# Performance work log

Hardware: AMD Instinct MI355X
Metric: run time of the kernel (lower is better)

Reference implementation:

```python
import jax, jax.numpy as jnp
import numpy as np

NUM_EXPERTS = 8
TOP_K = 2
HIDDEN = 768
FFN = 3072
B, S = 4, 4096


def setup_inputs() -> dict:
    key = jax.random.key(0)
    ks = jax.random.split(key, 7)
    scale_h = 1.0 / np.sqrt(HIDDEN)
    scale_f = 1.0 / np.sqrt(FFN)
    return {
        "hidden_states": jax.random.normal(ks[0], (B, S, HIDDEN), dtype=jnp.float32),
        "router_w": jax.random.normal(ks[1], (HIDDEN, NUM_EXPERTS), dtype=jnp.float32) * scale_h,
        "router_b": jnp.zeros((NUM_EXPERTS,), dtype=jnp.float32),
        "w1": jax.random.normal(ks[2], (NUM_EXPERTS, HIDDEN, FFN), dtype=jnp.float32) * scale_h,
        "b1": jnp.zeros((NUM_EXPERTS, FFN), dtype=jnp.float32),
        "w2": jax.random.normal(ks[3], (NUM_EXPERTS, FFN, HIDDEN), dtype=jnp.float32) * scale_f,
        "b2": jnp.zeros((NUM_EXPERTS, HIDDEN), dtype=jnp.float32),
    }


def _moe_forward(x_flat, router_w, router_b, w1, b1, w2, b2):
    T = x_flat.shape[0]
    # Router: logits [T, E]
    router_logits = x_flat @ router_w + router_b
    routing_weights = jax.nn.softmax(router_logits, axis=-1)
    # Top-k gating: softmax over the selected top-k logits
    top_vals, top_idx = jax.lax.top_k(router_logits, TOP_K)
    top_gates = jax.nn.softmax(top_vals, axis=-1)
    # Scatter gates into dense dispatch mask [T, E]
    rows = jnp.arange(T)[:, None]
    dispatch_mask = jnp.zeros_like(routing_weights).at[rows, top_idx].set(top_gates)
    # Expert computation: combined = sum_e gate[:, e] * FFN_e(x)
    # (tokens with zero gate contribute exactly 0, matching the torch scatter-combine)
    combined = jnp.zeros_like(x_flat)
    for e in range(NUM_EXPERTS):
        h = jax.nn.gelu(x_flat @ w1[e] + b1[e])  # [T, FFN]
        y = h @ w2[e] + b2[e]                    # [T, HIDDEN]
        combined = combined + dispatch_mask[:, e:e + 1] * y
    # Auxiliary load-balancing loss
    mean_routing_prob = jnp.mean(routing_weights, axis=0)
    tokens_per_expert = jnp.sum(dispatch_mask, axis=0) / T
    aux_loss = jnp.sum(mean_routing_prob * tokens_per_expert) * NUM_EXPERTS
    return combined, routing_weights, dispatch_mask, aux_loss, router_logits


def reference(hidden_states, router_w, router_b, w1, b1, w2, b2):
    batch, seq, hid = hidden_states.shape
    x_flat = hidden_states.reshape(-1, hid)
    combined, routing_weights, dispatch_mask, aux_loss, router_logits = _moe_forward(
        x_flat, router_w, router_b, w1, b1, w2, b2)
    E = NUM_EXPERTS
    return (
        combined.reshape(batch, seq, hid),            # expert_outputs
        routing_weights.reshape(batch, seq, E),       # routing_weights
        dispatch_mask.reshape(batch, seq, E),         # dispatch_mask
        aux_loss,                                     # aux_loss
        router_logits.reshape(batch, seq, E),         # router_logits
    )
```

## Files before the change

kernel.cpp:

```cpp
#include <hip/hip_runtime.h>
#include <math.h>

#define TOKENS 16384
#define HID 768
#define FFN_DIM 3072
#define NEXP 8
#define MAX_TILES 264

#define RT_TPB 128
#define RT_BLOCKS (TOKENS / RT_TPB)

typedef __bf16 bf16x8 __attribute__((ext_vector_type(8)));
typedef float f32x4 __attribute__((ext_vector_type(4)));

#define GLOBAL_AS(p) ((const __attribute__((address_space(1))) void*)(p))
#define LDS_AS(p)    ((__attribute__((address_space(3))) void*)(p))

__device__ __forceinline__ float gelu_f(float x) {
    const float x3 = x * x * x;
    const float z = 0.7978845608028654f * (x + 0.044715f * x3);
    const float e = __expf(2.f * z);
    const float t = 1.f - 2.f / (e + 1.f);
    return 0.5f * x * (1.f + t);
}

__device__ __forceinline__ unsigned short f2bf(float v) {
    return __builtin_bit_cast(unsigned short, (__bf16)v);
}

__global__ void __launch_bounds__(512) router_kernel(
    const float* __restrict__ x, const float* __restrict__ rw,
    const float* __restrict__ rb,
    float* __restrict__ out_rw, float* __restrict__ out_dm,
    float* __restrict__ out_logits,
    int* __restrict__ counts, float* __restrict__ probsum,
    float* __restrict__ gatesum, int* __restrict__ lists,
    float* __restrict__ glists)
{
    __shared__ int s_cnt[NEXP], s_base[NEXP];
    __shared__ float s_prob[NEXP], s_gate[NEXP];
    __shared__ int s_e1[RT_TPB], s_s1[RT_TPB], s_e2[RT_TPB], s_s2[RT_TPB];
    __shared__ float s_g1v[RT_TPB], s_g2v[RT_TPB];

    const int tid = threadIdx.x;
    if (tid < NEXP) { s_cnt[tid] = 0; s_prob[tid] = 0.f; s_gate[tid] = 0.f; }
    __syncthreads();

    const int wave = tid >> 6, lane = tid & 63;

    for (int it = 0; it < RT_TPB / 8; ++it) {
        const int lt = wave * (RT_TPB / 8) + it;
        const int t = blockIdx.x * RT_TPB + lt;
        const float* xr = x + (size_t)t * HID;
        float acc[NEXP];
#pragma unroll
        for (int e = 0; e < NEXP; ++e) acc[e] = 0.f;
#pragma unroll
        for (int j = 0; j < 12; ++j) {
            const int i = lane + (j << 6);
            const float xv = xr[i];
            const float4 a = ((const float4*)(rw + (size_t)i * NEXP))[0];
            const float4 b = ((const float4*)(rw + (size_t)i * NEXP))[1];
            acc[0] += xv * a.x; acc[1] += xv * a.y; acc[2] += xv * a.z; acc[3] += xv * a.w;
            acc[4] += xv * b.x; acc[5] += xv * b.y; acc[6] += xv * b.z; acc[7] += xv * b.w;
        }
#pragma unroll
        for (int off = 32; off > 0; off >>= 1)
#pragma unroll
            for (int e = 0; e < NEXP; ++e) acc[e] += __shfl_down(acc[e], off, 64);

        if (lane == 0) {
            float lg[NEXP];
            float m = -1e30f;
#pragma unroll
            for (int e = 0; e < NEXP; ++e) { lg[e] = acc[e] + rb[e]; m = fmaxf(m, lg[e]); }
            float ex[NEXP]; float s = 0.f;
#pragma unroll
            for (int e = 0; e < NEXP; ++e) { ex[e] = expf(lg[e] - m); s += ex[e]; }
            const float inv = 1.f / s;
            float* lrow = out_logits + (size_t)t * NEXP;
            float* prow = out_rw + (size_t)t * NEXP;
#pragma unroll
            for (int e = 0; e < NEXP; ++e) {
                lrow[e] = lg[e];
                const float p = ex[e] * inv;
                prow[e] = p;
                atomicAdd(&s_prob[e], p);
            }
            int i1 = 0;
#pragma unroll
            for (int e = 1; e < NEXP; ++e) if (lg[e] > lg[i1]) i1 = e;
            int i2 = (i1 == 0) ? 1 : 0;
#pragma unroll
            for (int e = 0; e < NEXP; ++e) if (e != i1 && lg[e] > lg[i2]) i2 = e;
            const float e2 = expf(lg[i2] - lg[i1]);
            const float g1 = 1.f / (1.f + e2);
            const float g2 = e2 / (1.f + e2);
            out_dm[(size_t)t * NEXP + i1] = g1;
            out_dm[(size_t)t * NEXP + i2] = g2;
            atomicAdd(&s_gate[i1], g1);
            atomicAdd(&s_gate[i2], g2);
            s_e1[lt] = i1; s_s1[lt] = atomicAdd(&s_cnt[i1], 1); s_g1v[lt] = g1;
            s_e2[lt] = i2; s_s2[lt] = atomicAdd(&s_cnt[i2], 1); s_g2v[lt] = g2;
        }
    }
    __syncthreads();
    if (tid < NEXP) {
        s_base[tid] = atomicAdd(&counts[tid], s_cnt[tid]);
        atomicAdd(&probsum[tid], s_prob[tid]);
        atomicAdd(&gatesum[tid], s_gate[tid]);
    }
    __syncthreads();
    if (tid < RT_TPB) {
        const int t = blockIdx.x * RT_TPB + tid;
        int e = s_e1[tid]; int p = s_base[e] + s_s1[tid];
        lists[e * TOKENS + p] = t; glists[e * TOKENS + p] = s_g1v[tid];
        e = s_e2[tid]; p = s_base[e] + s_s2[tid];
        lists[e * TOKENS + p] = t; glists[e * TOKENS + p] = s_g2v[tid];
    }
}

__global__ void finalize_kernel(const int* __restrict__ counts,
                                const float* __restrict__ probsum,
                                const float* __restrict__ gatesum,
                                int* __restrict__ poffs,
                                float* __restrict__ out_aux)
{
    if (threadIdx.x == 0 && blockIdx.x == 0) {
        float s = 0.f; int po = 0;
        for (int e = 0; e < NEXP; ++e) {
            poffs[e] = po;
            po += ((counts[e] + 127) >> 7) << 7;
            s += (probsum[e] / (float)TOKENS) * (gatesum[e] / (float)TOKENS);
        }
        poffs[NEXP] = po;
        *out_aux = s * (float)NEXP;
    }
}

__global__ void __launch_bounds__(192) gatherx_kernel(
    const float* __restrict__ x, const int* __restrict__ counts,
    const int* __restrict__ poffs, const int* __restrict__ lists,
    unsigned short* __restrict__ Xg)
{
    const int r = blockIdx.x;
    if (r >= poffs[NEXP]) return;
    int e = 0;
#pragma unroll
    for (int q = 1; q < NEXP; ++q) e += (r >= poffs[q]);
    const int ri = r - poffs[e];
    const int tid = threadIdx.x;
    uint2 o = make_uint2(0u, 0u);
    if (ri < counts[e]) {
        const int tok = lists[e * TOKENS + ri];
        const float4 v = *(const float4*)&x[(size_t)tok * HID + tid * 4];
        o.x = (unsigned)f2bf(v.x) | ((unsigned)f2bf(v.y) << 16);
        o.y = (unsigned)f2bf(v.z) | ((unsigned)f2bf(v.w) << 16);
    }
    *(uint2*)&Xg[(size_t)r * HID + tid * 4] = o;
}

__global__ void __launch_bounds__(256) convT_kernel(const float* __restrict__ in,
                                                    unsigned short* __restrict__ out,
                                                    int R, int C)
{
    __shared__ float sT[32][65];
    const int e = blockIdx.z;
    const float* in_e = in + (size_t)e * R * C;
    unsigned short* out_e = out + (size_t)e * R * C;
    const int r0 = blockIdx.y * 64;
    const int c0 = blockIdx.x * 32;
    const int tid = threadIdx.x;
    const int rr = tid >> 3, c4 = (tid & 7) * 4;
#pragma unroll
    for (int half = 0; half < 2; ++half) {
        const int r = rr + half * 32;
        const float4 v = *(const float4*)&in_e[(size_t)(r0 + r) * C + c0 + c4];
        sT[c4 + 0][r] = v.x; sT[c4 + 1][r] = v.y;
        sT[c4 + 2][r] = v.z; sT[c4 + 3][r] = v.w;
    }
    __syncthreads();
    const int c = tid >> 3, u = tid & 7;
    uint4 pk;
    const float* sr = &sT[c][u * 8];
    pk.x = (unsigned)f2bf(sr[0]) | ((unsigned)f2bf(sr[1]) << 16);
    pk.y = (unsigned)f2bf(sr[2]) | ((unsigned)f2bf(sr[3]) << 16);
    pk.z = (unsigned)f2bf(sr[4]) | ((unsigned)f2bf(sr[5]) << 16);
    pk.w = (unsigned)f2bf(sr[6]) | ((unsigned)f2bf(sr[7]) << 16);
    *(uint4*)&out_e[(size_t)(c0 + c) * R + r0 + u * 8] = pk;
}

__global__ void __launch_bounds__(256) gemm1_kernel(
    const unsigned short* __restrict__ Xg, const unsigned short* __restrict__ W1T,
    const float* __restrict__ b1, const int* __restrict__ poffs,
    unsigned short* __restrict__ H, int grBase, int tilesPG)
{
    const int mtile = blockIdx.x;
    if (mtile >= tilesPG) return;
    const int gr = grBase + mtile * 128;
    if (gr >= poffs[NEXP]) return;
    int e = 0;
#pragma unroll
    for (int q = 1; q < NEXP; ++q) e += (gr >= poffs[q]);
    const int hbase = gr - grBase;
    const int n0 = blockIdx.y * 128;

    __shared__ __bf16 sA[128 * 64];
    __shared__ __bf16 sB[128 * 64];

    const int tid = threadIdx.x;
    const int w = tid >> 6, lane = tid & 63;

    const unsigned short* w1e = W1T + (size_t)e * (FFN_DIM * HID);
    const int lr = lane >> 3;
    const int lk = (lane & 7) * 8;
    const unsigned short* aPtr[4];
    const unsigned short* bPtr[4];
    __bf16* ldsA[4];
    __bf16* ldsB[4];
#pragma unroll
    for (int j = 0; j < 4; ++j) {
        const int row = (w * 4 + j) * 8 + lr;
        aPtr[j] = Xg + (size_t)(gr + row) * HID + lk;
        bPtr[j] = w1e + (size_t)(n0 + row) * HID + lk;
        ldsA[j] = sA + (w * 4 + j) * 512;
        ldsB[j] = sB + (w * 4 + j) * 512;
    }

    f32x4 acc[4][4];
#pragma unroll
    for (int a = 0; a < 4; ++a)
#pragma unroll
        for (int b = 0; b < 4; ++b) acc[a][b] = (f32x4)(0.f);

    const int wm = (w >> 1) * 64, wn = (w & 1) * 64;
    const int fr = lane & 15;
    const int fk = (lane >> 4) * 8;

    for (int kt = 0; kt < HID / 64; ++kt) {
        const int k0 = kt * 64;
#pragma unroll
        for (int j = 0; j < 4; ++j) {
            __builtin_amdgcn_global_load_lds(GLOBAL_AS(aPtr[j] + k0), LDS_AS(ldsA[j]), 16, 0, 0);
            __builtin_amdgcn_global_load_lds(GLOBAL_AS(bPtr[j] + k0), LDS_AS(ldsB[j]), 16, 0, 0);
        }
        __syncthreads();
#pragma unroll
        for (int kk = 0; kk < 64; kk += 32) {
            bf16x8 af[4], bb[4];
#pragma unroll
            for (int t = 0; t < 4; ++t) {
                af[t] = *(const bf16x8*)&sA[(wm + t * 16 + fr) * 64 + kk + fk];
                bb[t] = *(const bf16x8*)&sB[(wn + t * 16 + fr) * 64 + kk + fk];
            }
#pragma unroll
            for (int tm = 0; tm < 4; ++tm)
#pragma unroll
                for (int tn = 0; tn < 4; ++tn)
                    acc[tm][tn] = __builtin_amdgcn_mfma_f32_16x16x32_bf16(
                        af[tm], bb[tn], acc[tm][tn], 0, 0, 0);
        }
        __syncthreads();
    }

    const float* b1e = b1 + (size_t)e * FFN_DIM;
    float bias[4];
#pragma unroll
    for (int tn = 0; tn < 4; ++tn) bias[tn] = b1e[n0 + wn + tn * 16 + fr];
#pragma unroll
    for (int tm = 0; tm < 4; ++tm) {
#pragma unroll
        for (int tn = 0; tn < 4; ++tn) {
            const int n = n0 + wn + tn * 16 + fr;
#pragma unroll
            for (int r = 0; r < 4; ++r) {
                const int mloc = wm + tm * 16 + (lane >> 4) * 4 + r;
                const float h = gelu_f(acc[tm][tn][r] + bias[tn]);
                H[(size_t)(hbase + mloc) * FFN_DIM + n] = f2bf(h);
            }
        }
    }
}

__global__ void __launch_bounds__(256) gemm2_kernel(
    const unsigned short* __restrict__ H, const unsigned short* __restrict__ W2T,
    const float* __restrict__ b2, const int* __restrict__ counts,
    const int* __restrict__ poffs, const int* __restrict__ lists,
    const float* __restrict__ glists, float* __restrict__ out,
    int grBase, int tilesPG)
{
    const int mtile = blockIdx.x;
    if (mtile >= tilesPG) return;
    const int gr = grBase + mtile * 128;
    if (gr >= poffs[NEXP]) return;
    int e = 0;
#pragma unroll
    for (int q = 1; q < NEXP; ++q) e += (gr >= poffs[q]);
    const int cnt = counts[e];
    const int m0 = gr - poffs[e];
    const int hbase = gr - grBase;
    const int n0 = blockIdx.y * 128;

    __shared__ __bf16 sA[128 * 64];
    __shared__ __bf16 sB[128 * 64];
    __shared__ int sTok[128];
    __shared__ float sGate[128];

    const int tid = threadIdx.x;
    const int w = tid >> 6, lane = tid & 63;
    if (tid < 128) {
        int ri = m0 + tid; if (ri > cnt - 1) ri = cnt - 1;
        sTok[tid] = lists[e * TOKENS + ri];
        sGate[tid] = glists[e * TOKENS + ri];
    }

    const unsigned short* w2e = W2T + (size_t)e * (FFN_DIM * HID);
    const int lr = lane >> 3;
    const int lk = (lane & 7) * 8;
    const unsigned short* aPtr[4];
    const unsigned short* bPtr[4];
    __bf16* ldsA[4];
    __bf16* ldsB[4];
#pragma unroll
    for (int j = 0; j < 4; ++j) {
        const int row = (w * 4 + j) * 8 + lr;
        aPtr[j] = H + (size_t)(hbase + row) * FFN_DIM + lk;
        bPtr[j] = w2e + (size_t)(n0 + row) * FFN_DIM + lk;
        ldsA[j] = sA + (w * 4 + j) * 512;
        ldsB[j] = sB + (w * 4 + j) * 512;
    }

    f32x4 acc[4][4];
#pragma unroll
    for (int a = 0; a < 4; ++a)
#pragma unroll
        for (int b = 0; b < 4; ++b) acc[a][b] = (f32x4)(0.f);

    const int wm = (w >> 1) * 64, wn = (w & 1) * 64;
    const int fr = lane & 15;
    const int fk = (lane >> 4) * 8;

    for (int kt = 0; kt < FFN_DIM / 64; ++kt) {
        const int k0 = kt * 64;
#pragma unroll
        for (int j = 0; j < 4; ++j) {
            __builtin_amdgcn_global_load_lds(GLOBAL_AS(aPtr[j] + k0), LDS_AS(ldsA[j]), 16, 0, 0);
            __builtin_amdgcn_global_load_lds(GLOBAL_AS(bPtr[j] + k0), LDS_AS(ldsB[j]), 16, 0, 0);
        }
        __syncthreads();
#pragma unroll
        for (int kk = 0; kk < 64; kk += 32) {
            bf16x8 af[4], bb[4];
#pragma unroll
            for (int t = 0; t < 4; ++t) {
                af[t] = *(const bf16x8*)&sA[(wm + t * 16 + fr) * 64 + kk + fk];
                bb[t] = *(const bf16x8*)&sB[(wn + t * 16 + fr) * 64 + kk + fk];
            }
#pragma unroll
            for (int tm = 0; tm < 4; ++tm)
#pragma unroll
                for (int tn = 0; tn < 4; ++tn)
                    acc[tm][tn] = __builtin_amdgcn_mfma_f32_16x16x32_bf16(
                        af[tm], bb[tn], acc[tm][tn], 0, 0, 0);
        }
        __syncthreads();
    }

    const float* b2e = b2 + (size_t)e * HID;
    float bias[4];
#pragma unroll
    for (int tn = 0; tn < 4; ++tn) bias[tn] = b2e[n0 + wn + tn * 16 + fr];
#pragma unroll
    for (int tm = 0; tm < 4; ++tm) {
#pragma unroll
        for (int tn = 0; tn < 4; ++tn) {
            const int n = n0 + wn + tn * 16 + fr;
#pragma unroll
            for (int r = 0; r < 4; ++r) {
                const int mloc = wm + tm * 16 + (lane >> 4) * 4 + r;
                if (m0 + mloc < cnt) {
                    const float y = acc[tm][tn][r] + bias[tn];
                    atomicAdd(&out[(size_t)sTok[mloc] * HID + n], sGate[mloc] * y);
                }
            }
        }
    }
}

#define BM 16
#define KC 64
#define XS 772
#define HS 68
__global__ void __launch_bounds__(256) ffn_kernel(
    const float* __restrict__ x, const float* __restrict__ w1,
    const float* __restrict__ b1, const float* __restrict__ w2,
    const float* __restrict__ b2, const int* __restrict__ counts,
    const int* __restrict__ lists, const float* __restrict__ glists,
    float* __restrict__ out)
{
    const int e = blockIdx.y;
    const int count = counts[e];
    const int row0 = blockIdx.x * BM;
    if (row0 >= count) return;

    __shared__ float sX[BM * XS];
    __shared__ float sH[BM * HS];
    __shared__ int sTokF[BM];
    __shared__ float sGateF[BM];
    const int tid = threadIdx.x;

    if (tid < BM) {
        const int ri = row0 + tid;
        int tok = 0; float g = 0.f;
        if (ri < count) { tok = lists[e * TOKENS + ri]; g = glists[e * TOKENS + ri]; }
        sTokF[tid] = tok; sGateF[tid] = g;
    }
    __syncthreads();
    {
        const int r = tid >> 4, q = tid & 15;
        const float4* src = (const float4*)(x + (size_t)sTokF[r] * HID);
#pragma unroll
        for (int j = 0; j < 12; ++j) {
            const float4 v = src[q + (j << 4)];
            *(float4*)&sX[r * XS + ((q + (j << 4)) << 2)] = v;
        }
    }
    __syncthreads();

    const float* w1e = w1 + (size_t)e * HID * FFN_DIM;
    const float* w2e = w2 + (size_t)e * FFN_DIM * HID;
    const float* b1e = b1 + (size_t)e * FFN_DIM;
    const float* b2e = b2 + (size_t)e * HID;
    const int r1 = tid & 15;
    const int c0 = (tid >> 4) << 2;
    const int c2 = (tid >> 4) * 48;

    float Y[48];
#pragma unroll
    for (int j = 0; j < 48; ++j) Y[j] = 0.f;

    for (int ch = 0; ch < FFN_DIM / KC; ++ch) {
        float h0 = 0.f, h1 = 0.f, h2 = 0.f, h3 = 0.f;
        const float* w1c = w1e + ch * KC + c0;
        for (int i = 0; i < HID; i += 4) {
            const float4 xv = *(const float4*)&sX[r1 * XS + i];
            const float* wp = w1c + (size_t)i * FFN_DIM;
            const float4 wa = *(const float4*)(wp);
            const float4 wb = *(const float4*)(wp + FFN_DIM);
            const float4 wc = *(const float4*)(wp + 2 * FFN_DIM);
            const float4 wd = *(const float4*)(wp + 3 * FFN_DIM);
            h0 += xv.x * wa.x + xv.y * wb.x + xv.z * wc.x + xv.w * wd.x;
            h1 += xv.x * wa.y + xv.y * wb.y + xv.z * wc.y + xv.w * wd.y;
            h2 += xv.x * wa.z + xv.y * wb.z + xv.z * wc.z + xv.w * wd.z;
            h3 += xv.x * wa.w + xv.y * wb.w + xv.z * wc.w + xv.w * wd.w;
        }
        const int cb = ch * KC + c0;
        h0 = gelu_f(h0 + b1e[cb + 0]);
        h1 = gelu_f(h1 + b1e[cb + 1]);
        h2 = gelu_f(h2 + b1e[cb + 2]);
        h3 = gelu_f(h3 + b1e[cb + 3]);
        __syncthreads();
        *(float4*)&sH[r1 * HS + c0] = make_float4(h0, h1, h2, h3);
        __syncthreads();
        const float* w2c = w2e + (size_t)ch * KC * HID + c2;
        for (int k = 0; k < KC; ++k) {
            const float hv = sH[r1 * HS + k];
            const float4* wr = (const float4*)(w2c + (size_t)k * HID);
#pragma unroll
            for (int j4 = 0; j4 < 12; ++j4) {
                const float4 wv = wr[j4];
                Y[j4 * 4 + 0] += hv * wv.x;
                Y[j4 * 4 + 1] += hv * wv.y;
                Y[j4 * 4 + 2] += hv * wv.z;
                Y[j4 * 4 + 3] += hv * wv.w;
            }
        }
    }
    const int ri = row0 + r1;
    if (ri < count) {
        const float g = sGateF[r1];
        float* orow = out + (size_t)sTokF[r1] * HID + c2;
#pragma unroll
        for (int j = 0; j < 48; ++j)
            atomicAdd(&orow[j], g * (Y[j] + b2e[c2 + j]));
    }
}

extern "C" void kernel_launch(void* const* d_in, const int* in_sizes, int n_in,
                              void* d_out, int out_size, void* d_ws, size_t ws_size,
                              hipStream_t stream)
{
    const float* x  = (const float*)d_in[0];
    const float* rw = (const float*)d_in[1];
    const float* rb = (const float*)d_in[2];
    const float* w1 = (const float*)d_in[3];
    const float* b1 = (const float*)d_in[4];
    const float* w2 = (const float*)d_in[5];
    const float* b2 = (const float*)d_in[6];

    float* out = (float*)d_out;
    float* out_comb   = out;
    float* out_rw     = out + (size_t)TOKENS * HID;
    float* out_dm     = out_rw + (size_t)TOKENS * NEXP;
    float* out_aux    = out_dm + (size_t)TOKENS * NEXP;
    float* out_logits = out_aux + 1;

    char* ws = (char*)d_ws;
    int*   counts  = (int*)ws;
    int*   poffs   = (int*)(ws + 64);
    float* probsum = (float*)(ws + 128);
    float* gatesum = (float*)(ws + 160);
    int*   lists   = (int*)(ws + 256);
    float* glists  = (float*)(ws + 256 + (size_t)NEXP * TOKENS * 4);
    size_t off = 256 + (size_t)NEXP * TOKENS * 8;
    off = (off + 255) & ~(size_t)255;
    unsigned short* Xg  = (unsigned short*)(ws + off); off += (size_t)MAX_TILES * 128 * HID * 2;
    unsigned short* W1T = (unsigned short*)(ws + off); off += (size_t)NEXP * HID * FFN_DIM * 2;
    unsigned short* W2T = (unsigned short*)(ws + off); off += (size_t)NEXP * HID * FFN_DIM * 2;
    unsigned short* Hbuf = (unsigned short*)(ws + off);
    const size_t fixed = off;

    int G = -1, tilesPG = 0;
    const int cand[6] = {1, 2, 4, 8, 16, 32};
    for (int ci = 0; ci < 6; ++ci) {
        const int g = cand[ci];
        const int t = (MAX_TILES + g - 1) / g;
        const size_t need = fixed + (size_t)t * 128 * FFN_DIM * 2;
        if (need <= ws_size) { G = g; tilesPG = t; break; }
    }

    hipMemsetAsync(out_comb, 0, (size_t)TOKENS * HID * sizeof(float), stream);
    hipMemsetAsync(out_dm, 0, (size_t)TOKENS * NEXP * sizeof(float), stream);
    hipMemsetAsync(d_ws, 0, 256, stream);

    router_kernel<<<dim3(RT_BLOCKS), 512, 0, stream>>>(
        x, rw, rb, out_rw, out_dm, out_logits,
        counts, probsum, gatesum, lists, glists);
    finalize_kernel<<<1, 64, 0, stream>>>(counts, probsum, gatesum, poffs, out_aux);

    if (G > 0) {
        gatherx_kernel<<<dim3(MAX_TILES * 128), 192, 0, stream>>>(
            x, counts, poffs, lists, Xg);
        convT_kernel<<<dim3(FFN_DIM / 32, HID / 64, NEXP), 256, 0, stream>>>(w1, W1T, HID, FFN_DIM);
        convT_kernel<<<dim3(HID / 32, FFN_DIM / 64, NEXP), 256, 0, stream>>>(w2, W2T, FFN_DIM, HID);
        const int mtPad = (tilesPG + 7) & ~7;
        for (int g = 0; g < G; ++g) {
            const int grBase = g * tilesPG * 128;
            gemm1_kernel<<<dim3(mtPad, FFN_DIM / 128), 256, 0, stream>>>(
                Xg, W1T, b1, poffs, Hbuf, grBase, tilesPG);
            gemm2_kernel<<<dim3(mtPad, HID / 128), 256, 0, stream>>>(
                Hbuf, W2T, b2, counts, poffs, lists, glists, out_comb, grBase, tilesPG);
        }
    } else {
        ffn_kernel<<<dim3(TOKENS / BM, NEXP), 256, 0, stream>>>(
            x, w1, b1, w2, b2, counts, lists, glists, out_comb);
    }
}
```

Before: 1.010 ms.

## Enlarge expert GEMM tiles to 256x128 with triple-buffered swizzled LDS pipeline

```diff
diff --git a/kernel.cpp b/kernel.cpp
--- a/kernel.cpp
+++ b/kernel.cpp
@@ -5,7 +5,7 @@
 #define HID 768
 #define FFN_DIM 3072
 #define NEXP 8
-#define MAX_TILES 264
+#define MAXT 136
 
 #define RT_TPB 128
 #define RT_BLOCKS (TOKENS / RT_TPB)
@@ -15,6 +15,7 @@
 
 #define GLOBAL_AS(p) ((const __attribute__((address_space(1))) void*)(p))
 #define LDS_AS(p)    ((__attribute__((address_space(3))) void*)(p))
+#define SB0 __builtin_amdgcn_sched_barrier(0)
 
 __device__ __forceinline__ float gelu_f(float x) {
     const float x3 = x * x * x;
@@ -130,7 +131,7 @@
         float s = 0.f; int po = 0;
         for (int e = 0; e < NEXP; ++e) {
             poffs[e] = po;
-            po += ((counts[e] + 127) >> 7) << 7;
+            po += ((counts[e] + 255) >> 8) << 8;
             s += (probsum[e] / (float)TOKENS) * (gatesum[e] / (float)TOKENS);
         }
         poffs[NEXP] = po;
@@ -190,108 +191,137 @@
     *(uint4*)&out_e[(size_t)(c0 + c) * R + r0 + u * 8] = pk;
 }
 
-__global__ void __launch_bounds__(256) gemm1_kernel(
+
+#define STAGE_AB(os_, kt_) do {                                                                          \
+    const unsigned short* _a = aSrc + (kt_) * 64;                                                        \
+    const unsigned short* _b = bSrc + (kt_) * 64;                                                        \
+    __builtin_amdgcn_global_load_lds(GLOBAL_AS(_a + (size_t)(wv*32 +  0) * KS), LDS_AS(&lds[(os_) +         (wv*32 +  0) * 64]), 16, 0, 0); \
+    __builtin_amdgcn_global_load_lds(GLOBAL_AS(_a + (size_t)(wv*32 +  8) * KS), LDS_AS(&lds[(os_) +         (wv*32 +  8) * 64]), 16, 0, 0); \
+    __builtin_amdgcn_global_load_lds(GLOBAL_AS(_a + (size_t)(wv*32 + 16) * KS), LDS_AS(&lds[(os_) +         (wv*32 + 16) * 64]), 16, 0, 0); \
+    __builtin_amdgcn_global_load_lds(GLOBAL_AS(_a + (size_t)(wv*32 + 24) * KS), LDS_AS(&lds[(os_) +         (wv*32 + 24) * 64]), 16, 0, 0); \
+    __builtin_amdgcn_global_load_lds(GLOBAL_AS(_b + (size_t)(wv*16 +  0) * KS), LDS_AS(&lds[(os_) + 16384 + (wv*16 +  0) * 64]), 16, 0, 0); \
+    __builtin_amdgcn_global_load_lds(GLOBAL_AS(_b + (size_t)(wv*16 +  8) * KS), LDS_AS(&lds[(os_) + 16384 + (wv*16 +  8) * 64]), 16, 0, 0); \
+} while (0)
+
+#define DECODE_TILE(NT_) \
+    const int nwg = gridDim.x;                                                       \
+    const int orig = blockIdx.x;                                                     \
+    const int qq = nwg >> 3, rr2 = nwg & 7;                                          \
+    const int xcd = orig & 7, pos = orig >> 3;                                       \
+    const int wid = (xcd < rr2 ? xcd * (qq + 1) : rr2 * (qq + 1) + (xcd - rr2) * qq) + pos; \
+    const int nSuper = tilesPG >> 3;                                                 \
+    const int fullB = nSuper * 8 * (NT_);                                            \
+    int mt, nti;                                                                     \
+    if (wid < fullB) {                                                               \
+        const int st = wid / (8 * (NT_));                                            \
+        const int lo = wid - st * (8 * (NT_));                                       \
+        mt = (st << 3) + (lo & 7);                                                   \
+        nti = lo >> 3;                                                               \
+    } else {                                                                         \
+        const int rem = tilesPG - (nSuper << 3);                                     \
+        const int lo = wid - fullB;                                                  \
+        mt = (nSuper << 3) + lo % rem;                                               \
+        nti = lo / rem;                                                              \
+    }
+
+__global__ void __launch_bounds__(512, 2) gemm1_kernel(
     const unsigned short* __restrict__ Xg, const unsigned short* __restrict__ W1T,
     const float* __restrict__ b1, const int* __restrict__ poffs,
     unsigned short* __restrict__ H, int grBase, int tilesPG)
 {
-    const int mtile = blockIdx.x;
-    if (mtile >= tilesPG) return;
-    const int gr = grBase + mtile * 128;
+    extern __shared__ __bf16 lds[];
+    const int KS = HID;
+    const int NK = HID / 64;
+
+    DECODE_TILE(FFN_DIM / 128)
+    const int gr = grBase + mt * 256;
     if (gr >= poffs[NEXP]) return;
     int e = 0;
 #pragma unroll
     for (int q = 1; q < NEXP; ++q) e += (gr >= poffs[q]);
     const int hbase = gr - grBase;
-    const int n0 = blockIdx.y * 128;
-
-    __shared__ __bf16 sA[128 * 64];
-    __shared__ __bf16 sB[128 * 64];
+    const int n0 = nti * 128;
 
     const int tid = threadIdx.x;
-    const int w = tid >> 6, lane = tid & 63;
-
-    const unsigned short* w1e = W1T + (size_t)e * (FFN_DIM * HID);
-    const int lr = lane >> 3;
-    const int lk = (lane & 7) * 8;
-    const unsigned short* aPtr[4];
-    const unsigned short* bPtr[4];
-    __bf16* ldsA[4];
-    __bf16* ldsB[4];
-#pragma unroll
-    for (int j = 0; j < 4; ++j) {
-        const int row = (w * 4 + j) * 8 + lr;
-        aPtr[j] = Xg + (size_t)(gr + row) * HID + lk;
-        bPtr[j] = w1e + (size_t)(n0 + row) * HID + lk;
-        ldsA[j] = sA + (w * 4 + j) * 512;
-        ldsB[j] = sB + (w * 4 + j) * 512;
-    }
-
-    f32x4 acc[4][4];
-#pragma unroll
-    for (int a = 0; a < 4; ++a)
-#pragma unroll
-        for (int b = 0; b < 4; ++b) acc[a][b] = (f32x4)(0.f);
-
-    const int wm = (w >> 1) * 64, wn = (w & 1) * 64;
-    const int fr = lane & 15;
-    const int fk = (lane >> 4) * 8;
-
-    for (int kt = 0; kt < HID / 64; ++kt) {
-        const int k0 = kt * 64;
-#pragma unroll
-        for (int j = 0; j < 4; ++j) {
-            __builtin_amdgcn_global_load_lds(GLOBAL_AS(aPtr[j] + k0), LDS_AS(ldsA[j]), 16, 0, 0);
-            __builtin_amdgcn_global_load_lds(GLOBAL_AS(bPtr[j] + k0), LDS_AS(ldsB[j]), 16, 0, 0);
-        }
-        __syncthreads();
-#pragma unroll
-        for (int kk = 0; kk < 64; kk += 32) {
-            bf16x8 af[4], bb[4];
-#pragma unroll
-            for (int t = 0; t < 4; ++t) {
-                af[t] = *(const bf16x8*)&sA[(wm + t * 16 + fr) * 64 + kk + fk];
-                bb[t] = *(const bf16x8*)&sB[(wn + t * 16 + fr) * 64 + kk + fk];
-            }
-#pragma unroll
-            for (int tm = 0; tm < 4; ++tm)
-#pragma unroll
-                for (int tn = 0; tn < 4; ++tn)
-                    acc[tm][tn] = __builtin_amdgcn_mfma_f32_16x16x32_bf16(
-                        af[tm], bb[tn], acc[tm][tn], 0, 0, 0);
-        }
-        __syncthreads();
+    const int wv = tid >> 6, lane = tid & 63;
+    const int wr = wv >> 2, wc = wv & 3;
+    const int fr = lane & 15, q4 = lane >> 4, sw = fr & 7;
+    const int rlo = lane >> 3;
+    const int cswz = ((lane & 7) ^ rlo) << 3;
+
+    const unsigned short* aSrc = Xg + (size_t)(gr + rlo) * KS + cswz;
+    const unsigned short* bSrc = W1T + (size_t)e * (HID * FFN_DIM) + (size_t)(n0 + rlo) * KS + cswz;
+
+    const int aRow = (wr * 128 + fr) * 64;
+    const int bRow = (wc * 32 + fr) * 64;
+    const int c0 = (q4 ^ sw) << 3;
+    const int c1 = ((4 + q4) ^ sw) << 3;
+
+    f32x4 acc[8][2];
+#pragma unroll
+    for (int i = 0; i < 8; ++i) { acc[i][0] = (f32x4)(0.f); acc[i][1] = (f32x4)(0.f); }
+
+    int oc = 0, on = 24576, os = 49152;
+    STAGE_AB(oc, 0);
+    STAGE_AB(on, 1);
+    asm volatile("s_waitcnt vmcnt(6)" ::: "memory");
+    SB0; __builtin_amdgcn_s_barrier(); SB0;
+
+    for (int kt = 0; kt < NK; ++kt) {
+        if (kt + 2 < NK) STAGE_AB(os, kt + 2);
+        __builtin_amdgcn_s_setprio(1);
+        const bf16x8 b00 = *(const bf16x8*)&lds[oc + 16384 + bRow + c0];
+        const bf16x8 b01 = *(const bf16x8*)&lds[oc + 16384 + bRow + c1];
+        const bf16x8 b10 = *(const bf16x8*)&lds[oc + 16384 + bRow + 1024 + c0];
+        const bf16x8 b11 = *(const bf16x8*)&lds[oc + 16384 + bRow + 1024 + c1];
+#pragma unroll
+        for (int mi = 0; mi < 8; ++mi) {
+            const bf16x8 a0 = *(const bf16x8*)&lds[oc + aRow + mi * 1024 + c0];
+            const bf16x8 a1 = *(const bf16x8*)&lds[oc + aRow + mi * 1024 + c1];
+            acc[mi][0] = __builtin_amdgcn_mfma_f32_16x16x32_bf16(a0, b00, acc[mi][0], 0, 0, 0);
+            acc[mi][0] = __builtin_amdgcn_mfma_f32_16x16x32_bf16(a1, b01, acc[mi][0], 0, 0, 0);
+            acc[mi][1] = __builtin_amdgcn_mfma_f32_16x16x32_bf16(a0, b10, acc[mi][1], 0, 0, 0);
+            acc[mi][1] = __builtin_amdgcn_mfma_f32_16x16x32_bf16(a1, b11, acc[mi][1], 0, 0, 0);
+        }
+        __builtin_amdgcn_s_setprio(0);
+        if (kt + 1 < NK) {
+            SB0;
+            if (kt + 2 < NK) asm volatile("s_waitcnt vmcnt(6)" ::: "memory");
+            else             asm volatile("s_waitcnt vmcnt(0)" ::: "memory");
+            __builtin_amdgcn_s_barrier(); SB0;
+        }
+        const int t_ = oc; oc = on; on = os; os = t_;
     }
 
     const float* b1e = b1 + (size_t)e * FFN_DIM;
-    float bias[4];
-#pragma unroll
-    for (int tn = 0; tn < 4; ++tn) bias[tn] = b1e[n0 + wn + tn * 16 + fr];
-#pragma unroll
-    for (int tm = 0; tm < 4; ++tm) {
-#pragma unroll
-        for (int tn = 0; tn < 4; ++tn) {
-            const int n = n0 + wn + tn * 16 + fr;
-#pragma unroll
-            for (int r = 0; r < 4; ++r) {
-                const int mloc = wm + tm * 16 + (lane >> 4) * 4 + r;
-                const float h = gelu_f(acc[tm][tn][r] + bias[tn]);
-                H[(size_t)(hbase + mloc) * FFN_DIM + n] = f2bf(h);
-            }
-        }
-    }
-}
-
-__global__ void __launch_bounds__(256) gemm2_kernel(
+    const float bias0 = b1e[n0 + wc * 32 + fr];
+    const float bias1 = b1e[n0 + wc * 32 + 16 + fr];
+    unsigned short* Hcol = H + (size_t)hbase * FFN_DIM + n0 + wc * 32 + fr;
+#pragma unroll
+    for (int mi = 0; mi < 8; ++mi) {
+#pragma unroll
+        for (int r = 0; r < 4; ++r) {
+            const int m = wr * 128 + mi * 16 + q4 * 4 + r;
+            unsigned short* hp = Hcol + (size_t)m * FFN_DIM;
+            hp[0]  = f2bf(gelu_f(acc[mi][0][r] + bias0));
+            hp[16] = f2bf(gelu_f(acc[mi][1][r] + bias1));
+        }
+    }
+}
+
+__global__ void __launch_bounds__(512, 2) gemm2_kernel(
     const unsigned short* __restrict__ H, const unsigned short* __restrict__ W2T,
     const float* __restrict__ b2, const int* __restrict__ counts,
     const int* __restrict__ poffs, const int* __restrict__ lists,
     const float* __restrict__ glists, float* __restrict__ out,
     int grBase, int tilesPG)
 {
-    const int mtile = blockIdx.x;
-    if (mtile >= tilesPG) return;
-    const int gr = grBase + mtile * 128;
+    extern __shared__ __bf16 lds[];
+    const int KS = FFN_DIM;
+    const int NK = FFN_DIM / 64;
+
+    DECODE_TILE(HID / 128)
+    const int gr = grBase + mt * 256;
     if (gr >= poffs[NEXP]) return;
     int e = 0;
 #pragma unroll
@@ -299,89 +329,82 @@
     const int cnt = counts[e];
     const int m0 = gr - poffs[e];
     const int hbase = gr - grBase;
-    const int n0 = blockIdx.y * 128;
-
-    __shared__ __bf16 sA[128 * 64];
-    __shared__ __bf16 sB[128 * 64];
-    __shared__ int sTok[128];
-    __shared__ float sGate[128];
+    const int n0 = nti * 128;
 
     const int tid = threadIdx.x;
-    const int w = tid >> 6, lane = tid & 63;
-    if (tid < 128) {
+    const int wv = tid >> 6, lane = tid & 63;
+    const int wr = wv >> 2, wc = wv & 3;
+    const int fr = lane & 15, q4 = lane >> 4, sw = fr & 7;
+    const int rlo = lane >> 3;
+    const int cswz = ((lane & 7) ^ rlo) << 3;
+
+    const unsigned short* aSrc = H + (size_t)(hbase + rlo) * KS + cswz;
+    const unsigned short* bSrc = W2T + (size_t)e * (HID * FFN_DIM) + (size_t)(n0 + rlo) * KS + cswz;
+
+    const int aRow = (wr * 128 + fr) * 64;
+    const int bRow = (wc * 32 + fr) * 64;
+    const int c0 = (q4 ^ sw) << 3;
+    const int c1 = ((4 + q4) ^ sw) << 3;
+
+    f32x4 acc[8][2];
+#pragma unroll
+    for (int i = 0; i < 8; ++i) { acc[i][0] = (f32x4)(0.f); acc[i][1] = (f32x4)(0.f); }
+
+    int oc = 0, on = 24576, os = 49152;
+    STAGE_AB(oc, 0);
+    STAGE_AB(on, 1);
+    asm volatile("s_waitcnt vmcnt(6)" ::: "memory");
+    SB0; __builtin_amdgcn_s_barrier(); SB0;
+
+    for (int kt = 0; kt < NK; ++kt) {
+        if (kt + 2 < NK) STAGE_AB(os, kt + 2);
+        __builtin_amdgcn_s_setprio(1);
+        const bf16x8 b00 = *(const bf16x8*)&lds[oc + 16384 + bRow + c0];
+        const bf16x8 b01 = *(const bf16x8*)&lds[oc + 16384 + bRow + c1];
+        const bf16x8 b10 = *(const bf16x8*)&lds[oc + 16384 + bRow + 1024 + c0];
+        const bf16x8 b11 = *(const bf16x8*)&lds[oc + 16384 + bRow + 1024 + c1];
+#pragma unroll
+        for (int mi = 0; mi < 8; ++mi) {
+            const bf16x8 a0 = *(const bf16x8*)&lds[oc + aRow + mi * 1024 + c0];
+            const bf16x8 a1 = *(const bf16x8*)&lds[oc + aRow + mi * 1024 + c1];
+            acc[mi][0] = __builtin_amdgcn_mfma_f32_16x16x32_bf16(a0, b00, acc[mi][0], 0, 0, 0);
+            acc[mi][0] = __builtin_amdgcn_mfma_f32_16x16x32_bf16(a1, b01, acc[mi][0], 0, 0, 0);
+            acc[mi][1] = __builtin_amdgcn_mfma_f32_16x16x32_bf16(a0, b10, acc[mi][1], 0, 0, 0);
+            acc[mi][1] = __builtin_amdgcn_mfma_f32_16x16x32_bf16(a1, b11, acc[mi][1], 0, 0, 0);
+        }
+        __builtin_amdgcn_s_setprio(0);
+        if (kt + 1 < NK) {
+            SB0;
+            if (kt + 2 < NK) asm volatile("s_waitcnt vmcnt(6)" ::: "memory");
+            else             asm volatile("s_waitcnt vmcnt(0)" ::: "memory");
+            __builtin_amdgcn_s_barrier(); SB0;
+        }
+        const int t_ = oc; oc = on; on = os; os = t_;
+    }
+
+    int* sTok = (int*)(lds + 73728);
+    float* sGate = (float*)(lds + 73728 + 512);
+    if (tid < 256) {
         int ri = m0 + tid; if (ri > cnt - 1) ri = cnt - 1;
         sTok[tid] = lists[e * TOKENS + ri];
         sGate[tid] = glists[e * TOKENS + ri];
     }
-
-    const unsigned short* w2e = W2T + (size_t)e * (FFN_DIM * HID);
-    const int lr = lane >> 3;
-    const int lk = (lane & 7) * 8;
-    const unsigned short* aPtr[4];
-    const unsigned short* bPtr[4];
-    __bf16* ldsA[4];
-    __bf16* ldsB[4];
-#pragma unroll
-    for (int j = 0; j < 4; ++j) {
-        const int row = (w * 4 + j) * 8 + lr;
-        aPtr[j] = H + (size_t)(hbase + row) * FFN_DIM + lk;
-        bPtr[j] = w2e + (size_t)(n0 + row) * FFN_DIM + lk;
-        ldsA[j] = sA + (w * 4 + j) * 512;
-        ldsB[j] = sB + (w * 4 + j) * 512;
-    }
-
-    f32x4 acc[4][4];
-#pragma unroll
-    for (int a = 0; a < 4; ++a)
-#pragma unroll
-        for (int b = 0; b < 4; ++b) acc[a][b] = (f32x4)(0.f);
-
-    const int wm = (w >> 1) * 64, wn = (w & 1) * 64;
-    const int fr = lane & 15;
-    const int fk = (lane >> 4) * 8;
-
-    for (int kt = 0; kt < FFN_DIM / 64; ++kt) {
-        const int k0 = kt * 64;
-#pragma unroll
-        for (int j = 0; j < 4; ++j) {
-            __builtin_amdgcn_global_load_lds(GLOBAL_AS(aPtr[j] + k0), LDS_AS(ldsA[j]), 16, 0, 0);
-            __builtin_amdgcn_global_load_lds(GLOBAL_AS(bPtr[j] + k0), LDS_AS(ldsB[j]), 16, 0, 0);
-        }
-        __syncthreads();
-#pragma unroll
-        for (int kk = 0; kk < 64; kk += 32) {
-            bf16x8 af[4], bb[4];
-#pragma unroll
-            for (int t = 0; t < 4; ++t) {
-                af[t] = *(const bf16x8*)&sA[(wm + t * 16 + fr) * 64 + kk + fk];
-                bb[t] = *(const bf16x8*)&sB[(wn + t * 16 + fr) * 64 + kk + fk];
-            }
-#pragma unroll
-            for (int tm = 0; tm < 4; ++tm)
-#pragma unroll
-                for (int tn = 0; tn < 4; ++tn)
-                    acc[tm][tn] = __builtin_amdgcn_mfma_f32_16x16x32_bf16(
-                        af[tm], bb[tn], acc[tm][tn], 0, 0, 0);
-        }
-        __syncthreads();
-    }
+    __syncthreads();
 
     const float* b2e = b2 + (size_t)e * HID;
-    float bias[4];
-#pragma unroll
-    for (int tn = 0; tn < 4; ++tn) bias[tn] = b2e[n0 + wn + tn * 16 + fr];
-#pragma unroll
-    for (int tm = 0; tm < 4; ++tm) {
-#pragma unroll
-        for (int tn = 0; tn < 4; ++tn) {
-            const int n = n0 + wn + tn * 16 + fr;
-#pragma unroll
-            for (int r = 0; r < 4; ++r) {
-                const int mloc = wm + tm * 16 + (lane >> 4) * 4 + r;
-                if (m0 + mloc < cnt) {
-                    const float y = acc[tm][tn][r] + bias[tn];
-                    atomicAdd(&out[(size_t)sTok[mloc] * HID + n], sGate[mloc] * y);
-                }
+    const float bias0 = b2e[n0 + wc * 32 + fr];
+    const float bias1 = b2e[n0 + wc * 32 + 16 + fr];
+#pragma unroll
+    for (int mi = 0; mi < 8; ++mi) {
+#pragma unroll
+        for (int r = 0; r < 4; ++r) {
+            const int m = wr * 128 + mi * 16 + q4 * 4 + r;
+            if (m0 + m < cnt) {
+                const int tok = sTok[m];
+                const float g = sGate[m];
+                float* orow = out + (size_t)tok * HID + n0 + wc * 32 + fr;
+                atomicAdd(orow,      g * (acc[mi][0][r] + bias0));
+                atomicAdd(orow + 16, g * (acc[mi][1][r] + bias1));
             }
         }
     }
@@ -514,19 +537,17 @@
     float* glists  = (float*)(ws + 256 + (size_t)NEXP * TOKENS * 4);
     size_t off = 256 + (size_t)NEXP * TOKENS * 8;
     off = (off + 255) & ~(size_t)255;
-    unsigned short* Xg  = (unsigned short*)(ws + off); off += (size_t)MAX_TILES * 128 * HID * 2;
+    unsigned short* Xg  = (unsigned short*)(ws + off); off += (size_t)MAXT * 256 * HID * 2;
     unsigned short* W1T = (unsigned short*)(ws + off); off += (size_t)NEXP * HID * FFN_DIM * 2;
     unsigned short* W2T = (unsigned short*)(ws + off); off += (size_t)NEXP * HID * FFN_DIM * 2;
     unsigned short* Hbuf = (unsigned short*)(ws + off);
-    const size_t fixed = off;
-
-    int G = -1, tilesPG = 0;
-    const int cand[6] = {1, 2, 4, 8, 16, 32};
-    for (int ci = 0; ci < 6; ++ci) {
-        const int g = cand[ci];
-        const int t = (MAX_TILES + g - 1) / g;
-        const size_t need = fixed + (size_t)t * 128 * FFN_DIM * 2;
-        if (need <= ws_size) { G = g; tilesPG = t; break; }
+
+    size_t avail = (ws_size > off) ? (ws_size - off) : 0;
+    const int tilesFit = (int)(avail / ((size_t)256 * FFN_DIM * 2));
+    int G = 0, tilesPG = 0;
+    if (tilesFit >= 1) {
+        G = (MAXT + tilesFit - 1) / tilesFit;
+        tilesPG = (MAXT + G - 1) / G;
     }
 
     hipMemsetAsync(out_comb, 0, (size_t)TOKENS * HID * sizeof(float), stream);
@@ -539,16 +560,23 @@
     finalize_kernel<<<1, 64, 0, stream>>>(counts, probsum, gatesum, poffs, out_aux);
 
     if (G > 0) {
-        gatherx_kernel<<<dim3(MAX_TILES * 128), 192, 0, stream>>>(
+        static int attr_done = 0;
+        if (!attr_done) {
+            hipFuncSetAttribute((const void*)gemm1_kernel,
+                                hipFuncAttributeMaxDynamicSharedMemorySize, 147456);
+            hipFuncSetAttribute((const void*)gemm2_kernel,
+                                hipFuncAttributeMaxDynamicSharedMemorySize, 149504);
+            attr_done = 1;
+        }
+        gatherx_kernel<<<dim3(MAXT * 256), 192, 0, stream>>>(
             x, counts, poffs, lists, Xg);
         convT_kernel<<<dim3(FFN_DIM / 32, HID / 64, NEXP), 256, 0, stream>>>(w1, W1T, HID, FFN_DIM);
         convT_kernel<<<dim3(HID / 32, FFN_DIM / 64, NEXP), 256, 0, stream>>>(w2, W2T, FFN_DIM, HID);
-        const int mtPad = (tilesPG + 7) & ~7;
         for (int g = 0; g < G; ++g) {
-            const int grBase = g * tilesPG * 128;
-            gemm1_kernel<<<dim3(mtPad, FFN_DIM / 128), 256, 0, stream>>>(
+            const int grBase = g * tilesPG * 256;
+            gemm1_kernel<<<dim3(tilesPG * (FFN_DIM / 128)), 512, 147456, stream>>>(
                 Xg, W1T, b1, poffs, Hbuf, grBase, tilesPG);
-            gemm2_kernel<<<dim3(mtPad, HID / 128), 256, 0, stream>>>(
+            gemm2_kernel<<<dim3(tilesPG * (HID / 128)), 512, 149504, stream>>>(
                 Hbuf, W2T, b2, counts, poffs, lists, glists, out_comb, grBase, tilesPG);
         }
     } else {
```

Measured after the change: 836.4 us. 1.21x faster.

## Swizzle LDS layout, remap grid for XCD locality, pad experts to 256

Applied to the files above, without the earlier changes.

```diff
diff --git a/kernel.cpp b/kernel.cpp
--- a/kernel.cpp
+++ b/kernel.cpp
@@ -5,7 +5,7 @@
 #define HID 768
 #define FFN_DIM 3072
 #define NEXP 8
-#define MAX_TILES 264
+#define MAXT 136
 
 #define RT_TPB 128
 #define RT_BLOCKS (TOKENS / RT_TPB)
@@ -130,7 +130,7 @@
         float s = 0.f; int po = 0;
         for (int e = 0; e < NEXP; ++e) {
             poffs[e] = po;
-            po += ((counts[e] + 127) >> 7) << 7;
+            po += ((counts[e] + 255) >> 8) << 8;
             s += (probsum[e] / (float)TOKENS) * (gatesum[e] / (float)TOKENS);
         }
         poffs[NEXP] = po;
@@ -190,42 +190,72 @@
     *(uint4*)&out_e[(size_t)(c0 + c) * R + r0 + u * 8] = pk;
 }
 
-__global__ void __launch_bounds__(256) gemm1_kernel(
+
+#define STAGE1(kt_) do { \
+    _Pragma("unroll") \
+    for (int _kh = 0; _kh < 2; ++_kh) { \
+        const unsigned short* _pa = aStP + (kt_) * 64 + _kh * 32; \
+        const unsigned short* _pb = bStP + (kt_) * 64 + _kh * 32; \
+        __builtin_amdgcn_global_load_lds(GLOBAL_AS(_pa),           LDS_AS(aD + _kh * 4096),       16, 0, 0); \
+        __builtin_amdgcn_global_load_lds(GLOBAL_AS(_pa + 16 * KS), LDS_AS(aD + _kh * 4096 + 512), 16, 0, 0); \
+        __builtin_amdgcn_global_load_lds(GLOBAL_AS(_pb),           LDS_AS(bD + _kh * 4096),       16, 0, 0); \
+        __builtin_amdgcn_global_load_lds(GLOBAL_AS(_pb + 16 * KS), LDS_AS(bD + _kh * 4096 + 512), 16, 0, 0); \
+    } \
+} while (0)
+
+#define DECODE_TILE(NT_, MT_) \
+    const int nwg = gridDim.x;                                                       \
+    const int orig = blockIdx.x;                                                     \
+    const int qq = nwg >> 3, rr2 = nwg & 7;                                          \
+    const int xcd = orig & 7, pos = orig >> 3;                                       \
+    const int wid = (xcd < rr2 ? xcd * (qq + 1) : rr2 * (qq + 1) + (xcd - rr2) * qq) + pos; \
+    const int nSuper = (MT_) >> 3;                                                   \
+    const int fullB = nSuper * 8 * (NT_);                                            \
+    int mt, nti;                                                                     \
+    if (wid < fullB) {                                                               \
+        const int st_ = wid / (8 * (NT_));                                           \
+        const int lo = wid - st_ * (8 * (NT_));                                      \
+        mt = (st_ << 3) + (lo & 7);                                                  \
+        nti = lo >> 3;                                                               \
+    } else {                                                                         \
+        const int rem = (MT_) - (nSuper << 3);                                       \
+        const int lo = wid - fullB;                                                  \
+        mt = (nSuper << 3) + lo % rem;                                               \
+        nti = lo / rem;                                                              \
+    }
+
+__global__ void __launch_bounds__(256, 3) gemm1_kernel(
     const unsigned short* __restrict__ Xg, const unsigned short* __restrict__ W1T,
     const float* __restrict__ b1, const int* __restrict__ poffs,
-    unsigned short* __restrict__ H, int grBase, int tilesPG)
-{
-    const int mtile = blockIdx.x;
-    if (mtile >= tilesPG) return;
-    const int gr = grBase + mtile * 128;
+    unsigned short* __restrict__ H, int grBase, int mtCount)
+{
+    __shared__ __bf16 sA[8192];
+    __shared__ __bf16 sB[8192];
+    const int KS = HID;
+    const int NKT = HID / 64;
+
+    DECODE_TILE(FFN_DIM / 128, mtCount)
+    const int gr = grBase + mt * 128;
     if (gr >= poffs[NEXP]) return;
     int e = 0;
 #pragma unroll
     for (int q = 1; q < NEXP; ++q) e += (gr >= poffs[q]);
     const int hbase = gr - grBase;
-    const int n0 = blockIdx.y * 128;
-
-    __shared__ __bf16 sA[128 * 64];
-    __shared__ __bf16 sB[128 * 64];
+    const int n0 = nti * 128;
 
     const int tid = threadIdx.x;
-    const int w = tid >> 6, lane = tid & 63;
-
-    const unsigned short* w1e = W1T + (size_t)e * (FFN_DIM * HID);
-    const int lr = lane >> 3;
-    const int lk = (lane & 7) * 8;
-    const unsigned short* aPtr[4];
-    const unsigned short* bPtr[4];
-    __bf16* ldsA[4];
-    __bf16* ldsB[4];
-#pragma unroll
-    for (int j = 0; j < 4; ++j) {
-        const int row = (w * 4 + j) * 8 + lr;
-        aPtr[j] = Xg + (size_t)(gr + row) * HID + lk;
-        bPtr[j] = w1e + (size_t)(n0 + row) * HID + lk;
-        ldsA[j] = sA + (w * 4 + j) * 512;
-        ldsB[j] = sB + (w * 4 + j) * 512;
-    }
+    const int wv = tid >> 6, lane = tid & 63;
+    const int wm = (wv >> 1) * 64, wn = (wv & 1) * 64;
+    const int fr = lane & 15, q4 = lane >> 4;
+    const int rowoff = lane >> 2;
+    const int swzW = ((lane & 3) ^ ((lane >> 3) & 3)) << 3;
+    const int swzR = (q4 ^ ((fr >> 1) & 3)) << 3;
+
+    const unsigned short* aStP = Xg + (size_t)(gr + wv * 32 + rowoff) * KS + swzW;
+    const unsigned short* bStP = W1T + (size_t)e * (HID * FFN_DIM)
+                               + (size_t)(n0 + wv * 32 + rowoff) * KS + swzW;
+    __bf16* aD = sA + wv * 1024;
+    __bf16* bD = sB + wv * 1024;
 
     f32x4 acc[4][4];
 #pragma unroll
@@ -233,25 +263,16 @@
 #pragma unroll
         for (int b = 0; b < 4; ++b) acc[a][b] = (f32x4)(0.f);
 
-    const int wm = (w >> 1) * 64, wn = (w & 1) * 64;
-    const int fr = lane & 15;
-    const int fk = (lane >> 4) * 8;
-
-    for (int kt = 0; kt < HID / 64; ++kt) {
-        const int k0 = kt * 64;
-#pragma unroll
-        for (int j = 0; j < 4; ++j) {
-            __builtin_amdgcn_global_load_lds(GLOBAL_AS(aPtr[j] + k0), LDS_AS(ldsA[j]), 16, 0, 0);
-            __builtin_amdgcn_global_load_lds(GLOBAL_AS(bPtr[j] + k0), LDS_AS(ldsB[j]), 16, 0, 0);
-        }
+    for (int kt = 0; kt < NKT; ++kt) {
+        STAGE1(kt);
         __syncthreads();
 #pragma unroll
-        for (int kk = 0; kk < 64; kk += 32) {
+        for (int kh = 0; kh < 2; ++kh) {
             bf16x8 af[4], bb[4];
 #pragma unroll
             for (int t = 0; t < 4; ++t) {
-                af[t] = *(const bf16x8*)&sA[(wm + t * 16 + fr) * 64 + kk + fk];
-                bb[t] = *(const bf16x8*)&sB[(wn + t * 16 + fr) * 64 + kk + fk];
+                af[t] = *(const bf16x8*)&sA[kh * 4096 + (wm + t * 16 + fr) * 32 + swzR];
+                bb[t] = *(const bf16x8*)&sB[kh * 4096 + (wn + t * 16 + fr) * 32 + swzR];
             }
 #pragma unroll
             for (int tm = 0; tm < 4; ++tm)
@@ -274,7 +295,7 @@
             const int n = n0 + wn + tn * 16 + fr;
 #pragma unroll
             for (int r = 0; r < 4; ++r) {
-                const int mloc = wm + tm * 16 + (lane >> 4) * 4 + r;
+                const int mloc = wm + tm * 16 + q4 * 4 + r;
                 const float h = gelu_f(acc[tm][tn][r] + bias[tn]);
                 H[(size_t)(hbase + mloc) * FFN_DIM + n] = f2bf(h);
             }
@@ -282,16 +303,22 @@
     }
 }
 
-__global__ void __launch_bounds__(256) gemm2_kernel(
+__global__ void __launch_bounds__(256, 3) gemm2_kernel(
     const unsigned short* __restrict__ H, const unsigned short* __restrict__ W2T,
     const float* __restrict__ b2, const int* __restrict__ counts,
     const int* __restrict__ poffs, const int* __restrict__ lists,
     const float* __restrict__ glists, float* __restrict__ out,
-    int grBase, int tilesPG)
-{
-    const int mtile = blockIdx.x;
-    if (mtile >= tilesPG) return;
-    const int gr = grBase + mtile * 128;
+    int grBase, int mtCount)
+{
+    __shared__ __bf16 sA[8192];
+    __shared__ __bf16 sB[8192];
+    __shared__ int sTok[128];
+    __shared__ float sGate[128];
+    const int KS = FFN_DIM;
+    const int NKT = FFN_DIM / 64;
+
+    DECODE_TILE(HID / 128, mtCount)
+    const int gr = grBase + mt * 128;
     if (gr >= poffs[NEXP]) return;
     int e = 0;
 #pragma unroll
@@ -299,36 +326,27 @@
     const int cnt = counts[e];
     const int m0 = gr - poffs[e];
     const int hbase = gr - grBase;
-    const int n0 = blockIdx.y * 128;
-
-    __shared__ __bf16 sA[128 * 64];
-    __shared__ __bf16 sB[128 * 64];
-    __shared__ int sTok[128];
-    __shared__ float sGate[128];
+    const int n0 = nti * 128;
 
     const int tid = threadIdx.x;
-    const int w = tid >> 6, lane = tid & 63;
+    const int wv = tid >> 6, lane = tid & 63;
+    const int wm = (wv >> 1) * 64, wn = (wv & 1) * 64;
+    const int fr = lane & 15, q4 = lane >> 4;
+    const int rowoff = lane >> 2;
+    const int swzW = ((lane & 3) ^ ((lane >> 3) & 3)) << 3;
+    const int swzR = (q4 ^ ((fr >> 1) & 3)) << 3;
+
     if (tid < 128) {
         int ri = m0 + tid; if (ri > cnt - 1) ri = cnt - 1;
         sTok[tid] = lists[e * TOKENS + ri];
         sGate[tid] = glists[e * TOKENS + ri];
     }
 
-    const unsigned short* w2e = W2T + (size_t)e * (FFN_DIM * HID);
-    const int lr = lane >> 3;
-    const int lk = (lane & 7) * 8;
-    const unsigned short* aPtr[4];
-    const unsigned short* bPtr[4];
-    __bf16* ldsA[4];
-    __bf16* ldsB[4];
-#pragma unroll
-    for (int j = 0; j < 4; ++j) {
-        const int row = (w * 4 + j) * 8 + lr;
-        aPtr[j] = H + (size_t)(hbase + row) * FFN_DIM + lk;
-        bPtr[j] = w2e + (size_t)(n0 + row) * FFN_DIM + lk;
-        ldsA[j] = sA + (w * 4 + j) * 512;
-        ldsB[j] = sB + (w * 4 + j) * 512;
-    }
+    const unsigned short* aStP = H + (size_t)(hbase + wv * 32 + rowoff) * KS + swzW;
+    const unsigned short* bStP = W2T + (size_t)e * (HID * FFN_DIM)
+                               + (size_t)(n0 + wv * 32 + rowoff) * KS + swzW;
+    __bf16* aD = sA + wv * 1024;
+    __bf16* bD = sB + wv * 1024;
 
     f32x4 acc[4][4];
 #pragma unroll
@@ -336,25 +354,16 @@
 #pragma unroll
         for (int b = 0; b < 4; ++b) acc[a][b] = (f32x4)(0.f);
 
-    const int wm = (w >> 1) * 64, wn = (w & 1) * 64;
-    const int fr = lane & 15;
-    const int fk = (lane >> 4) * 8;
-
-    for (int kt = 0; kt < FFN_DIM / 64; ++kt) {
-        const int k0 = kt * 64;
-#pragma unroll
-        for (int j = 0; j < 4; ++j) {
-            __builtin_amdgcn_global_load_lds(GLOBAL_AS(aPtr[j] + k0), LDS_AS(ldsA[j]), 16, 0, 0);
-            __builtin_amdgcn_global_load_lds(GLOBAL_AS(bPtr[j] + k0), LDS_AS(ldsB[j]), 16, 0, 0);
-        }
+    for (int kt = 0; kt < NKT; ++kt) {
+        STAGE1(kt);
         __syncthreads();
 #pragma unroll
-        for (int kk = 0; kk < 64; kk += 32) {
+        for (int kh = 0; kh < 2; ++kh) {
             bf16x8 af[4], bb[4];
 #pragma unroll
             for (int t = 0; t < 4; ++t) {
-                af[t] = *(const bf16x8*)&sA[(wm + t * 16 + fr) * 64 + kk + fk];
-                bb[t] = *(const bf16x8*)&sB[(wn + t * 16 + fr) * 64 + kk + fk];
+                af[t] = *(const bf16x8*)&sA[kh * 4096 + (wm + t * 16 + fr) * 32 + swzR];
+                bb[t] = *(const bf16x8*)&sB[kh * 4096 + (wn + t * 16 + fr) * 32 + swzR];
             }
 #pragma unroll
             for (int tm = 0; tm < 4; ++tm)
@@ -377,7 +386,7 @@
             const int n = n0 + wn + tn * 16 + fr;
 #pragma unroll
             for (int r = 0; r < 4; ++r) {
-                const int mloc = wm + tm * 16 + (lane >> 4) * 4 + r;
+                const int mloc = wm + tm * 16 + q4 * 4 + r;
                 if (m0 + mloc < cnt) {
                     const float y = acc[tm][tn][r] + bias[tn];
                     atomicAdd(&out[(size_t)sTok[mloc] * HID + n], sGate[mloc] * y);
@@ -514,19 +523,17 @@
     float* glists  = (float*)(ws + 256 + (size_t)NEXP * TOKENS * 4);
     size_t off = 256 + (size_t)NEXP * TOKENS * 8;
     off = (off + 255) & ~(size_t)255;
-    unsigned short* Xg  = (unsigned short*)(ws + off); off += (size_t)MAX_TILES * 128 * HID * 2;
+    unsigned short* Xg  = (unsigned short*)(ws + off); off += (size_t)MAXT * 256 * HID * 2;
     unsigned short* W1T = (unsigned short*)(ws + off); off += (size_t)NEXP * HID * FFN_DIM * 2;
     unsigned short* W2T = (unsigned short*)(ws + off); off += (size_t)NEXP * HID * FFN_DIM * 2;
     unsigned short* Hbuf = (unsigned short*)(ws + off);
-    const size_t fixed = off;
-
-    int G = -1, tilesPG = 0;
-    const int cand[6] = {1, 2, 4, 8, 16, 32};
-    for (int ci = 0; ci < 6; ++ci) {
-        const int g = cand[ci];
-        const int t = (MAX_TILES + g - 1) / g;
-        const size_t need = fixed + (size_t)t * 128 * FFN_DIM * 2;
-        if (need <= ws_size) { G = g; tilesPG = t; break; }
+
+    size_t avail = (ws_size > off) ? (ws_size - off) : 0;
+    const int tilesFit = (int)(avail / ((size_t)256 * FFN_DIM * 2));
+    int G = 0, tilesPG = 0;
+    if (tilesFit >= 1) {
+        G = (MAXT + tilesFit - 1) / tilesFit;
+        tilesPG = (MAXT + G - 1) / G;
     }
 
     hipMemsetAsync(out_comb, 0, (size_t)TOKENS * HID * sizeof(float), stream);
@@ -539,17 +546,17 @@
     finalize_kernel<<<1, 64, 0, stream>>>(counts, probsum, gatesum, poffs, out_aux);
 
     if (G > 0) {
-        gatherx_kernel<<<dim3(MAX_TILES * 128), 192, 0, stream>>>(
+        gatherx_kernel<<<dim3(MAXT * 256), 192, 0, stream>>>(
             x, counts, poffs, lists, Xg);
         convT_kernel<<<dim3(FFN_DIM / 32, HID / 64, NEXP), 256, 0, stream>>>(w1, W1T, HID, FFN_DIM);
         convT_kernel<<<dim3(HID / 32, FFN_DIM / 64, NEXP), 256, 0, stream>>>(w2, W2T, FFN_DIM, HID);
-        const int mtPad = (tilesPG + 7) & ~7;
         for (int g = 0; g < G; ++g) {
-            const int grBase = g * tilesPG * 128;
-            gemm1_kernel<<<dim3(mtPad, FFN_DIM / 128), 256, 0, stream>>>(
-                Xg, W1T, b1, poffs, Hbuf, grBase, tilesPG);
-            gemm2_kernel<<<dim3(mtPad, HID / 128), 256, 0, stream>>>(
-                Hbuf, W2T, b2, counts, poffs, lists, glists, out_comb, grBase, tilesPG);
+            const int grBase = g * tilesPG * 256;
+            const int mtCount = tilesPG * 2;
+            gemm1_kernel<<<dim3(mtCount * (FFN_DIM / 128)), 256, 0, stream>>>(
+                Xg, W1T, b1, poffs, Hbuf, grBase, mtCount);
+            gemm2_kernel<<<dim3(mtCount * (HID / 128)), 256, 0, stream>>>(
+                Hbuf, W2T, b2, counts, poffs, lists, glists, out_comb, grBase, mtCount);
         }
     } else {
         ffn_kernel<<<dim3(TOKENS / BM, NEXP), 256, 0, stream>>>(
```

Measured after the change: 838.8 us. 16.9% less time.
